# Optimization experiments

Measured on AMD Instinct MI355X. Metric: run time of the kernel, lower is better.

Reference implementation:

```python
import jax, jax.numpy as jnp
import numpy as np

B, T, DIM, H, DH, DT = 2, 2048, 1024, 16, 64, 32
Q_TEMP, K_TEMP = 1.0, 1.0
EPS = float(np.finfo(np.float32).eps)  # torch RMSNorm default eps for fp32
INV_SQRT_DH = 1.0 / np.sqrt(DH)


def _get_time(length, head_time_delta, time_angles, with_time_delta):
    # [T,1,1] positions, optionally offset per head -> [T,H,1]
    pos = jnp.arange(length, dtype=jnp.float32)[:, None, None]
    if with_time_delta:
        pos = pos + head_time_delta[None, :, None]          # [T,H,1]
    else:
        pos = jnp.broadcast_to(pos, (length, H, 1))          # [T,H,1]
    ang = pos * time_angles                                  # [T,H,Dt]
    c, s = jnp.cos(ang), jnp.sin(ang)
    return jnp.concatenate([c + s, c - s], axis=-1) * INV_SQRT_DH  # [T,H,2Dt]


def setup_inputs() -> dict:
    key = jax.random.key(0)
    ks = jax.random.split(key, 6)
    sc = 0.02
    states = jax.random.normal(ks[0], (B, T, DIM), jnp.float32)
    attention_mask = jnp.ones((B, T), jnp.int32)
    ln_w = jnp.ones((DIM,), jnp.float32)
    time_angles = 10000.0 ** (-1.0 / jnp.arange(1, DT + 1, dtype=jnp.float32))
    head_time_delta = jax.random.uniform(ks[1], (H,), jnp.float32)
    Wq = jax.random.normal(ks[2], (H * DH, DIM), jnp.float32) * sc
    q_bias = jnp.zeros((H * DH,), jnp.float32)
    Wk = jax.random.normal(ks[3], (H * DH, DIM), jnp.float32) * sc
    bk = jnp.zeros((H * DH,), jnp.float32)
    Wv = jax.random.normal(ks[4], (H * DH, DIM), jnp.float32) * sc
    bv = jnp.zeros((H * DH,), jnp.float32)
    Wo = jax.random.normal(ks[5], (DIM, H * DH), jnp.float32) * sc
    bo = jnp.zeros((DIM,), jnp.float32)
    return dict(states=states, attention_mask=attention_mask, ln_w=ln_w,
                time_angles=time_angles, head_time_delta=head_time_delta,
                Wq=Wq, q_bias=q_bias, Wk=Wk, bk=bk, Wv=Wv, bv=bv, Wo=Wo, bo=bo)


def reference(states, attention_mask, ln_w, time_angles, head_time_delta,
              Wq, q_bias, Wk, bk, Wv, bv, Wo, bo):
    # RMSNorm
    x = states * jax.lax.rsqrt(jnp.mean(states * states, axis=-1, keepdims=True) + EPS) * ln_w
    m = attention_mask.astype(x.dtype)[:, :, None, None]   # [B,T,1,1]

    # Q path -> q_attentioned [B,T,T,H]
    q = (x @ Wq.T - jnp.exp(q_bias)).reshape(B, T, H, DH)
    q_sm = jax.nn.softmax(q / Q_TEMP * m, axis=-1)
    t_q = _get_time(T, head_time_delta, time_angles, True)   # [T,H,2Dt]
    t_k = _get_time(T, head_time_delta, time_angles, False)  # [T,H,2Dt]
    q_timed = jnp.sum(q_sm, axis=-1, keepdims=True) * t_q    # [B,T,H,2Dt]
    q_att = jnp.einsum('bthd,lhd->btlh', q_timed, t_k)       # [B,T,T,H]

    # KV path
    k = (x @ Wk.T + bk).reshape(B, T, H, DH)
    k_sm = jax.nn.softmax(k / K_TEMP * m, axis=-1)
    v = (x @ Wv.T + bv).reshape(B, T, H, DH)
    kv = k_sm * v                                            # [B,T,H,Dh]

    loading = jnp.einsum('btlh,blhd->bthd', q_att, kv)       # [B,T,H,Dh]
    return loading.reshape(B, T, DIM) @ Wo.T + bo
```

## Files before the change

### kernel.cpp

```cpp
#include <hip/hip_runtime.h>
#include <math.h>

#define T_ 2048
#define H_ 16

typedef __attribute__((ext_vector_type(8))) short bfx8;
typedef __attribute__((ext_vector_type(4))) float f32x4;

__device__ __forceinline__ short f2bf(float f) {
  union { float f; unsigned u; } x; x.f = f;
  unsigned r = (x.u + 0x7FFFu + ((x.u >> 16) & 1u)) >> 16;
  return (short)r;
}
__device__ __forceinline__ float bf2f(short s) {
  union { unsigned u; float f; } x;
  x.u = ((unsigned)(unsigned short)s) << 16;
  return x.f;
}

#define GLD_LDS(g, l) \
  __builtin_amdgcn_global_load_lds( \
      (const __attribute__((address_space(1))) void*)(g), \
      (__attribute__((address_space(3))) void*)(l), 16, 0, 0)

__global__ __launch_bounds__(256) void prep_kernel(
    const float* __restrict__ Wk, const float* __restrict__ Wv,
    const float* __restrict__ Wo, const float* __restrict__ angles,
    const float* __restrict__ states, const float* __restrict__ ln_w,
    short* __restrict__ Wkb, short* __restrict__ Wvb, short* __restrict__ Wob,
    short* __restrict__ xb, short* __restrict__ Cb, short* __restrict__ tkT,
    float* __restrict__ MtH) {
  const int blk = blockIdx.x;
  if (blk < 3072) {
    const int i = blk * 256 + threadIdx.x;
    const int which = i >> 18;
    const int idx = i & 262143;
    const float* s = (which == 0) ? Wk : (which == 1) ? Wv : Wo;
    short* d = (which == 0) ? Wkb : (which == 1) ? Wvb : Wob;
    const float4 v = ((const float4*)s)[idx];
    short4 r;
    r.x = f2bf(v.x); r.y = f2bf(v.y); r.z = f2bf(v.z); r.w = f2bf(v.w);
    ((short4*)d)[idx] = r;
  } else if (blk < 7168) {
    const int row = blk - 3072;
    const int tid = threadIdx.x;
    const float4 v = ((const float4*)(states + (size_t)row * 1024))[tid];
    float ss = v.x * v.x + v.y * v.y + v.z * v.z + v.w * v.w;
#pragma unroll
    for (int off = 32; off >= 1; off >>= 1) ss += __shfl_xor(ss, off);
    __shared__ float red[4];
    if ((tid & 63) == 0) red[tid >> 6] = ss;
    __syncthreads();
    const float tot = red[0] + red[1] + red[2] + red[3];
    const float scale = rsqrtf(tot * (1.0f / 1024.0f) + 1.1920928955078125e-07f);
    const float4 w = ((const float4*)ln_w)[tid];
    short4 o;
    o.x = f2bf(v.x * scale * w.x);
    o.y = f2bf(v.y * scale * w.y);
    o.z = f2bf(v.z * scale * w.z);
    o.w = f2bf(v.w * scale * w.w);
    ((short4*)(xb + (size_t)row * 1024))[tid] = o;
  } else if (blk < 7424) {
    const int gid = (blk - 7168) * 256 + threadIdx.x;
    const int j = gid & 31;
    const int t = gid >> 5;
    float s, c;
    sincosf((float)t * angles[j], &s, &c);
    Cb[(size_t)t * 64 + j] = f2bf(0.125f * c);
    Cb[(size_t)t * 64 + 32 + j] = f2bf(0.125f * s);
  } else if (blk < 7456) {
    const int gid = (blk - 7424) * 256 + threadIdx.x;
    const int tc = gid & 255;
    const int j = gid >> 8;
    const float th = angles[j];
    short lo[8], hi[8];
#pragma unroll
    for (int r = 0; r < 8; ++r) {
      float s, c;
      sincosf((float)(tc * 8 + r) * th, &s, &c);
      lo[r] = f2bf((c + s) * 0.125f);
      hi[r] = f2bf((c - s) * 0.125f);
    }
    short* base = tkT + (size_t)j * 2048 + tc * 8;
    *(short4*)(base) = *(short4*)&lo[0];
    *(short4*)(base + 4) = *(short4*)&lo[4];
    short* base2 = tkT + (size_t)(32 + j) * 2048 + tc * 8;
    *(short4*)(base2) = *(short4*)&hi[0];
    *(short4*)(base2 + 4) = *(short4*)&hi[4];
  } else {
    const int gid = (blk - 7456) * 256 + threadIdx.x;
    ((float4*)MtH)[gid] = make_float4(0.f, 0.f, 0.f, 0.f);
  }
}

__global__ __launch_bounds__(256) void kvgemm_kernel(
    const short* __restrict__ xb, const short* __restrict__ Wkb,
    const short* __restrict__ Wvb, const float* __restrict__ bk,
    const float* __restrict__ bv, const int* __restrict__ mask,
    const short* __restrict__ tkT, float* __restrict__ Mt) {
  __shared__ short smem[16384];
  __shared__ short Vs[128][64];
  short(*As)[64] = (short(*)[64])smem;
  short(*Bk)[64] = (short(*)[64])(smem + 8192);
  short(*Bv)[64] = (short(*)[64])(smem + 12288);
  short(*kvS)[132] = (short(*)[132])smem;

  const int row0 = blockIdx.x * 128;
  const int h = blockIdx.y;
  const int t = threadIdx.x;
  const int lane = t & 63;
  const int wv = t >> 6;
  const bool isV = wv >= 2;
  const int wrow = (wv & 1) * 64;
  const int lrow = lane & 15;

  const int srow8 = t >> 3;
  const int kslotS = (t & 7) ^ (srow8 & 7);
  const short* gaS = xb + (size_t)(row0 + srow8) * 1024 + kslotS * 8;
  const short* gkS = Wkb + (size_t)(h * 64 + srow8) * 1024 + kslotS * 8;
  const short* gvS = Wvb + (size_t)(h * 64 + srow8) * 1024 + kslotS * 8;
  short* laS = &As[srow8][(t & 7) * 8];
  short* lkS = &Bk[srow8][(t & 7) * 8];
  short* lvS = &Bv[srow8][(t & 7) * 8];

  f32x4 acc[4][4] = {};
  for (int k0 = 0; k0 < 1024; k0 += 64) {
    GLD_LDS(gaS + k0, laS);
    GLD_LDS(gaS + 32 * 1024 + k0, laS + 2048);
    GLD_LDS(gaS + 64 * 1024 + k0, laS + 4096);
    GLD_LDS(gaS + 96 * 1024 + k0, laS + 6144);
    GLD_LDS(gkS + k0, lkS);
    GLD_LDS(gkS + 32 * 1024 + k0, lkS + 2048);
    GLD_LDS(gvS + k0, lvS);
    GLD_LDS(gvS + 32 * 1024 + k0, lvS + 2048);
    __syncthreads();
#pragma unroll
    for (int kk = 0; kk < 2; ++kk) {
      const int pcol = ((kk * 4 + (lane >> 4)) ^ (lrow & 7)) * 8;
      bfx8 af[4], bf_[4];
#pragma unroll
      for (int i = 0; i < 4; ++i)
        af[i] = *(const bfx8*)&As[wrow + i * 16 + lrow][pcol];
      const short(*Bs)[64] = isV ? Bv : Bk;
#pragma unroll
      for (int j = 0; j < 4; ++j)
        bf_[j] = *(const bfx8*)&Bs[j * 16 + lrow][pcol];
#pragma unroll
      for (int i = 0; i < 4; ++i)
#pragma unroll
        for (int j = 0; j < 4; ++j)
          acc[i][j] = __builtin_amdgcn_mfma_f32_16x16x32_bf16(af[i], bf_[j], acc[i][j], 0, 0, 0);
    }
    __syncthreads();
  }
  const int rq = (lane >> 4) * 4;
  if (isV) {
#pragma unroll
    for (int j = 0; j < 4; ++j) {
      const float bb = bv[h * 64 + j * 16 + lrow];
#pragma unroll
      for (int i = 0; i < 4; ++i)
#pragma unroll
        for (int rr = 0; rr < 4; ++rr)
          Vs[wrow + rq + i * 16 + rr][j * 16 + lrow] = f2bf(acc[i][j][rr] + bb);
    }
  }
  __syncthreads();
  if (!isV) {
    float bkc[4];
#pragma unroll
    for (int j = 0; j < 4; ++j) bkc[j] = bk[h * 64 + j * 16 + lrow];
    const int rowg0 = row0 + wrow + rq;
#pragma unroll
    for (int i = 0; i < 4; ++i) {
#pragma unroll
      for (int rr = 0; rr < 4; ++rr) {
        const float m = (float)mask[rowg0 + i * 16 + rr];
        float kf[4];
#pragma unroll
        for (int j = 0; j < 4; ++j) kf[j] = (acc[i][j][rr] + bkc[j]) * m;
        float mx = fmaxf(fmaxf(kf[0], kf[1]), fmaxf(kf[2], kf[3]));
#pragma unroll
        for (int off = 8; off >= 1; off >>= 1) mx = fmaxf(mx, __shfl_xor(mx, off));
        float s = 0.0f;
#pragma unroll
        for (int j = 0; j < 4; ++j) { kf[j] = expf(kf[j] - mx); s += kf[j]; }
#pragma unroll
        for (int off = 8; off >= 1; off >>= 1) s += __shfl_xor(s, off);
        const float inv = 1.0f / s;
#pragma unroll
        for (int j = 0; j < 4; ++j)
          acc[i][j][rr] = kf[j] * inv *
                          bf2f(Vs[wrow + rq + i * 16 + rr][j * 16 + lrow]);
      }
    }
#pragma unroll
    for (int j = 0; j < 4; ++j) {
      const int d = j * 16 + lrow;
#pragma unroll
      for (int i = 0; i < 4; ++i) {
        short4 o;
        o.x = f2bf(acc[i][j][0]); o.y = f2bf(acc[i][j][1]);
        o.z = f2bf(acc[i][j][2]); o.w = f2bf(acc[i][j][3]);
        *(short4*)&kvS[d][wrow + rq + i * 16] = o;
      }
    }
  }
  __syncthreads();
  const int bb = row0 >> 11;
  const int tb = row0 & 2047;
  const short* tkb = tkT + (size_t)(wv * 16 + lrow) * 2048 + tb;
  const int kg = (lane >> 4) * 8;
  f32x4 macc[4] = {};
#pragma unroll
  for (int kc = 0; kc < 4; ++kc) {
    const bfx8 af = *(const bfx8*)(tkb + kc * 32 + kg);
#pragma unroll
    for (int j = 0; j < 4; ++j) {
      const bfx8 bf_ = *(const bfx8*)&kvS[j * 16 + lrow][kc * 32 + kg];
      macc[j] = __builtin_amdgcn_mfma_f32_16x16x32_bf16(af, bf_, macc[j], 0, 0, 0);
    }
  }
  float* Mb = Mt + (size_t)(bb * 16 + h) * 4096;
#pragma unroll
  for (int j = 0; j < 4; ++j) {
    const int d = j * 16 + lrow;
#pragma unroll
    for (int rr = 0; rr < 4; ++rr) {
      const int e = wv * 16 + rq + rr;
      atomicAdd(&Mb[(size_t)e * 64 + d], macc[j][rr]);
    }
  }
}

__global__ __launch_bounds__(256) void fold_kernel(
    const float* __restrict__ Mt, const float* __restrict__ angles,
    const float* __restrict__ delta, short* __restrict__ Mf) {
  const int bh = blockIdx.x;
  const int b = bh >> 4, h = bh & 15;
  const int t = threadIdx.x;
  const int j = t >> 3;
  const int d8 = (t & 7) * 8;
  float sphi, cphi;
  sincosf(delta[h] * angles[j], &sphi, &cphi);
  const float p = cphi + sphi, q = cphi - sphi;
  const float* m0 = Mt + (size_t)bh * 4096 + (size_t)j * 64 + d8;
  const float* m1 = Mt + (size_t)bh * 4096 + (size_t)(32 + j) * 64 + d8;
  short* oc = Mf + (size_t)b * 65536 + (size_t)j * 1024 + h * 64 + d8;
  short* os = Mf + (size_t)b * 65536 + (size_t)(32 + j) * 1024 + h * 64 + d8;
#pragma unroll
  for (int c = 0; c < 8; ++c) {
    const float a = m0[c], bb = m1[c];
    oc[c] = f2bf(p * a + q * bb);
    os[c] = f2bf(q * a - p * bb);
  }
}

__global__ __launch_bounds__(256) void hgemm_kernel(
    const short* __restrict__ Wob, const short* __restrict__ Mf,
    float* __restrict__ H) {
  const int kc = blockIdx.x;
  const int o0 = blockIdx.y * 64;
  const int b = blockIdx.z;
  const int t = threadIdx.x;
  const int lane = t & 63;
  const int w = t >> 6;
  const int lrow = lane & 15;
  const int kg = (lane >> 4) * 8;
  const int orow = o0 + w * 16 + lrow;
  f32x4 acc[4] = {};
#pragma unroll
  for (int it = 0; it < 4; ++it) {
    const int kb = kc * 128 + it * 32 + kg;
    const bfx8 af = *(const bfx8*)(Wob + (size_t)orow * 1024 + kb);
#pragma unroll
    for (int j = 0; j < 4; ++j) {
      const bfx8 bf_ = *(const bfx8*)(Mf + (size_t)b * 65536 +
                                      (size_t)(j * 16 + lrow) * 1024 + kb);
      acc[j] = __builtin_amdgcn_mfma_f32_16x16x32_bf16(af, bf_, acc[j], 0, 0, 0);
    }
  }
  float* Hb = H + (size_t)b * 65536;
#pragma unroll
  for (int j = 0; j < 4; ++j) {
    const int kap = j * 16 + lrow;
#pragma unroll
    for (int rr = 0; rr < 4; ++rr) {
      const int o = o0 + w * 16 + (lane >> 4) * 4 + rr;
      atomicAdd(&Hb[(size_t)o * 64 + kap], acc[j][rr]);
    }
  }
}

__global__ __launch_bounds__(256) void ofinal_kernel(
    const short* __restrict__ Cb, const float* __restrict__ H,
    const float* __restrict__ bo, float* __restrict__ out) {
  const int col0 = blockIdx.x * 128;
  const int row0 = blockIdx.y * 128;
  const int b = blockIdx.z;
  float* C = out + (size_t)b * 2097152;
  const float* Hb = H + (size_t)b * 65536;
  const int t = threadIdx.x;
  const int lane = t & 63;
  const int wv = t >> 6;
  const int wm = (wv & 1) * 64, wn = (wv >> 1) * 64;
  const int lrow = lane & 15;
  const int kg = (lane >> 4) * 8;
  f32x4 acc[4][4] = {};
#pragma unroll
  for (int k0 = 0; k0 < 64; k0 += 32) {
    bfx8 af[4], bf_[4];
#pragma unroll
    for (int i = 0; i < 4; ++i)
      af[i] = *(const bfx8*)(Cb + (size_t)(row0 + wm + i * 16 + lrow) * 64 + k0 + kg);
#pragma unroll
    for (int j = 0; j < 4; ++j) {
      const float* hp = Hb + (size_t)(col0 + wn + j * 16 + lrow) * 64 + k0 + kg;
      const float4 h0 = *(const float4*)hp;
      const float4 h1 = *(const float4*)(hp + 4);
      bfx8 bb;
      bb[0] = f2bf(h0.x); bb[1] = f2bf(h0.y); bb[2] = f2bf(h0.z); bb[3] = f2bf(h0.w);
      bb[4] = f2bf(h1.x); bb[5] = f2bf(h1.y); bb[6] = f2bf(h1.z); bb[7] = f2bf(h1.w);
      bf_[j] = bb;
    }
#pragma unroll
    for (int i = 0; i < 4; ++i)
#pragma unroll
      for (int j = 0; j < 4; ++j)
        acc[i][j] = __builtin_amdgcn_mfma_f32_16x16x32_bf16(af[i], bf_[j], acc[i][j], 0, 0, 0);
  }
  const int rq = (lane >> 4) * 4;
#pragma unroll
  for (int j = 0; j < 4; ++j) {
    const int c = col0 + wn + j * 16 + lrow;
    const float bb = bo[c];
#pragma unroll
    for (int i = 0; i < 4; ++i) {
      const int r = row0 + wm + i * 16 + rq;
#pragma unroll
      for (int rr = 0; rr < 4; ++rr)
        C[(size_t)(r + rr) * 1024 + c] = acc[i][j][rr] + bb;
    }
  }
}

extern "C" void kernel_launch(void* const* d_in, const int* in_sizes, int n_in,
                              void* d_out, int out_size, void* d_ws, size_t ws_size,
                              hipStream_t stream) {
  (void)in_sizes; (void)n_in; (void)out_size; (void)ws_size;
  const float* states = (const float*)d_in[0];
  const int* mask = (const int*)d_in[1];
  const float* ln_w = (const float*)d_in[2];
  const float* angles = (const float*)d_in[3];
  const float* delta = (const float*)d_in[4];
  const float* Wk = (const float*)d_in[7];
  const float* bk = (const float*)d_in[8];
  const float* Wv = (const float*)d_in[9];
  const float* bv = (const float*)d_in[10];
  const float* Wo = (const float*)d_in[11];
  const float* bo = (const float*)d_in[12];
  float* out = (float*)d_out;

  char* W = (char*)d_ws;
  short* xb  = (short*)(W);
  short* Wkb = (short*)(W + (8u << 20));
  short* Wvb = (short*)(W + (10u << 20));
  short* Wob = (short*)(W + (12u << 20));
  short* Cb  = (short*)(W + (14u << 20));
  short* tkT = (short*)(W + (14u << 20) + (256u << 10));
  short* Mf  = (short*)(W + (14u << 20) + (512u << 10));
  float* Mt  = (float*)(W + (15u << 20));
  float* H   = (float*)(W + (15u << 20) + (512u << 10));

  prep_kernel<<<7712, 256, 0, stream>>>(Wk, Wv, Wo, angles, states, ln_w,
                                        Wkb, Wvb, Wob, xb, Cb, tkT, Mt);
  kvgemm_kernel<<<dim3(32, 16), 256, 0, stream>>>(xb, Wkb, Wvb, bk, bv, mask,
                                                  tkT, Mt);
  fold_kernel<<<32, 256, 0, stream>>>(Mt, angles, delta, Mf);
  hgemm_kernel<<<dim3(8, 16, 2), 256, 0, stream>>>(Wob, Mf, H);
  ofinal_kernel<<<dim3(8, 16, 2), 256, 0, stream>>>(Cb, H, bo, out);
}
```

Baseline: 146.9 us.

## Fuse kv-gemm, fold, H-gemm and output stages into one persistent kernel

Merges the four post-prep kernels into a single 512-block kernel with software grid barriers built on an atomic counter. The fold step is now done inline inside the H-gemm stage, so the Mf buffer round trip goes away, and the H and output stages are re-tiled to fit the fixed 512-block grid. This removes three launch gaps and one intermediate buffer. In exchange it adds spin-wait barriers that require every block to be co-resident, so the kernel could deadlock if occupancy is too low, and it adds a memset launch.

```diff
diff --git a/kernel.cpp b/kernel.cpp
--- a/kernel.cpp
+++ b/kernel.cpp
@@ -93,253 +93,287 @@
   }
 }
 
-__global__ __launch_bounds__(256) void kvgemm_kernel(
+__device__ __forceinline__ void grid_sync(int* cnt, int target) {
+  __syncthreads();
+  if (threadIdx.x == 0) {
+    __threadfence();
+    __hip_atomic_fetch_add(cnt, 1, __ATOMIC_ACQ_REL, __HIP_MEMORY_SCOPE_AGENT);
+    while (__hip_atomic_load(cnt, __ATOMIC_ACQUIRE, __HIP_MEMORY_SCOPE_AGENT) <
+           target)
+      __builtin_amdgcn_s_sleep(2);
+  }
+  __syncthreads();
+  __threadfence();
+}
+
+__global__ __launch_bounds__(256, 2) void fused_kernel(
     const short* __restrict__ xb, const short* __restrict__ Wkb,
     const short* __restrict__ Wvb, const float* __restrict__ bk,
     const float* __restrict__ bv, const int* __restrict__ mask,
-    const short* __restrict__ tkT, float* __restrict__ Mt) {
+    const short* __restrict__ tkT, float* __restrict__ Mt,
+    const short* __restrict__ Wob, const float* __restrict__ angles,
+    const float* __restrict__ delta, float* __restrict__ H,
+    const short* __restrict__ Cb, const float* __restrict__ bo,
+    float* __restrict__ out, int* __restrict__ cnt) {
   __shared__ short smem[16384];
   __shared__ short Vs[128][64];
-  short(*As)[64] = (short(*)[64])smem;
-  short(*Bk)[64] = (short(*)[64])(smem + 8192);
-  short(*Bv)[64] = (short(*)[64])(smem + 12288);
-  short(*kvS)[132] = (short(*)[132])smem;
-
-  const int row0 = blockIdx.x * 128;
-  const int h = blockIdx.y;
-  const int t = threadIdx.x;
-  const int lane = t & 63;
-  const int wv = t >> 6;
-  const bool isV = wv >= 2;
-  const int wrow = (wv & 1) * 64;
-  const int lrow = lane & 15;
-
-  const int srow8 = t >> 3;
-  const int kslotS = (t & 7) ^ (srow8 & 7);
-  const short* gaS = xb + (size_t)(row0 + srow8) * 1024 + kslotS * 8;
-  const short* gkS = Wkb + (size_t)(h * 64 + srow8) * 1024 + kslotS * 8;
-  const short* gvS = Wvb + (size_t)(h * 64 + srow8) * 1024 + kslotS * 8;
-  short* laS = &As[srow8][(t & 7) * 8];
-  short* lkS = &Bk[srow8][(t & 7) * 8];
-  short* lvS = &Bv[srow8][(t & 7) * 8];
-
-  f32x4 acc[4][4] = {};
-  for (int k0 = 0; k0 < 1024; k0 += 64) {
-    GLD_LDS(gaS + k0, laS);
-    GLD_LDS(gaS + 32 * 1024 + k0, laS + 2048);
-    GLD_LDS(gaS + 64 * 1024 + k0, laS + 4096);
-    GLD_LDS(gaS + 96 * 1024 + k0, laS + 6144);
-    GLD_LDS(gkS + k0, lkS);
-    GLD_LDS(gkS + 32 * 1024 + k0, lkS + 2048);
-    GLD_LDS(gvS + k0, lvS);
-    GLD_LDS(gvS + 32 * 1024 + k0, lvS + 2048);
+
+  {
+    short(*As)[64] = (short(*)[64])smem;
+    short(*Bk)[64] = (short(*)[64])(smem + 8192);
+    short(*Bv)[64] = (short(*)[64])(smem + 12288);
+    short(*kvS)[132] = (short(*)[132])smem;
+
+    const int row0 = (blockIdx.x & 31) * 128;
+    const int h = blockIdx.x >> 5;
+    const int t = threadIdx.x;
+    const int lane = t & 63;
+    const int wv = t >> 6;
+    const bool isV = wv >= 2;
+    const int wrow = (wv & 1) * 64;
+    const int lrow = lane & 15;
+
+    const int srow8 = t >> 3;
+    const int kslotS = (t & 7) ^ (srow8 & 7);
+    const short* gaS = xb + (size_t)(row0 + srow8) * 1024 + kslotS * 8;
+    const short* gkS = Wkb + (size_t)(h * 64 + srow8) * 1024 + kslotS * 8;
+    const short* gvS = Wvb + (size_t)(h * 64 + srow8) * 1024 + kslotS * 8;
+    short* laS = &As[srow8][(t & 7) * 8];
+    short* lkS = &Bk[srow8][(t & 7) * 8];
+    short* lvS = &Bv[srow8][(t & 7) * 8];
+
+    f32x4 acc[4][4] = {};
+    for (int k0 = 0; k0 < 1024; k0 += 64) {
+      GLD_LDS(gaS + k0, laS);
+      GLD_LDS(gaS + 32 * 1024 + k0, laS + 2048);
+      GLD_LDS(gaS + 64 * 1024 + k0, laS + 4096);
+      GLD_LDS(gaS + 96 * 1024 + k0, laS + 6144);
+      GLD_LDS(gkS + k0, lkS);
+      GLD_LDS(gkS + 32 * 1024 + k0, lkS + 2048);
+      GLD_LDS(gvS + k0, lvS);
+      GLD_LDS(gvS + 32 * 1024 + k0, lvS + 2048);
+      __syncthreads();
+#pragma unroll
+      for (int kk = 0; kk < 2; ++kk) {
+        const int pcol = ((kk * 4 + (lane >> 4)) ^ (lrow & 7)) * 8;
+        bfx8 af[4], bf_[4];
+#pragma unroll
+        for (int i = 0; i < 4; ++i)
+          af[i] = *(const bfx8*)&As[wrow + i * 16 + lrow][pcol];
+        const short(*Bs)[64] = isV ? Bv : Bk;
+#pragma unroll
+        for (int j = 0; j < 4; ++j)
+          bf_[j] = *(const bfx8*)&Bs[j * 16 + lrow][pcol];
+#pragma unroll
+        for (int i = 0; i < 4; ++i)
+#pragma unroll
+          for (int j = 0; j < 4; ++j)
+            acc[i][j] = __builtin_amdgcn_mfma_f32_16x16x32_bf16(af[i], bf_[j], acc[i][j], 0, 0, 0);
+      }
+      __syncthreads();
+    }
+    const int rq = (lane >> 4) * 4;
+    if (isV) {
+#pragma unroll
+      for (int j = 0; j < 4; ++j) {
+        const float bb = bv[h * 64 + j * 16 + lrow];
+#pragma unroll
+        for (int i = 0; i < 4; ++i)
+#pragma unroll
+          for (int rr = 0; rr < 4; ++rr)
+            Vs[wrow + rq + i * 16 + rr][j * 16 + lrow] = f2bf(acc[i][j][rr] + bb);
+      }
+    }
     __syncthreads();
-#pragma unroll
-    for (int kk = 0; kk < 2; ++kk) {
-      const int pcol = ((kk * 4 + (lane >> 4)) ^ (lrow & 7)) * 8;
-      bfx8 af[4], bf_[4];
-#pragma unroll
-      for (int i = 0; i < 4; ++i)
-        af[i] = *(const bfx8*)&As[wrow + i * 16 + lrow][pcol];
-      const short(*Bs)[64] = isV ? Bv : Bk;
-#pragma unroll
-      for (int j = 0; j < 4; ++j)
-        bf_[j] = *(const bfx8*)&Bs[j * 16 + lrow][pcol];
-#pragma unroll
-      for (int i = 0; i < 4; ++i)
+    if (!isV) {
+      float bkc[4];
+#pragma unroll
+      for (int j = 0; j < 4; ++j) bkc[j] = bk[h * 64 + j * 16 + lrow];
+      const int rowg0 = row0 + wrow + rq;
+#pragma unroll
+      for (int i = 0; i < 4; ++i) {
+#pragma unroll
+        for (int rr = 0; rr < 4; ++rr) {
+          const float m = (float)mask[rowg0 + i * 16 + rr];
+          float kf[4];
+#pragma unroll
+          for (int j = 0; j < 4; ++j) kf[j] = (acc[i][j][rr] + bkc[j]) * m;
+          float mx = fmaxf(fmaxf(kf[0], kf[1]), fmaxf(kf[2], kf[3]));
+#pragma unroll
+          for (int off = 8; off >= 1; off >>= 1) mx = fmaxf(mx, __shfl_xor(mx, off));
+          float s = 0.0f;
+#pragma unroll
+          for (int j = 0; j < 4; ++j) { kf[j] = expf(kf[j] - mx); s += kf[j]; }
+#pragma unroll
+          for (int off = 8; off >= 1; off >>= 1) s += __shfl_xor(s, off);
+          const float inv = 1.0f / s;
+#pragma unroll
+          for (int j = 0; j < 4; ++j)
+            acc[i][j][rr] = kf[j] * inv *
+                            bf2f(Vs[wrow + rq + i * 16 + rr][j * 16 + lrow]);
+        }
+      }
+#pragma unroll
+      for (int j = 0; j < 4; ++j) {
+        const int d = j * 16 + lrow;
+#pragma unroll
+        for (int i = 0; i < 4; ++i) {
+          short4 o;
+          o.x = f2bf(acc[i][j][0]); o.y = f2bf(acc[i][j][1]);
+          o.z = f2bf(acc[i][j][2]); o.w = f2bf(acc[i][j][3]);
+          *(short4*)&kvS[d][wrow + rq + i * 16] = o;
+        }
+      }
+    }
+    __syncthreads();
+    const int bb = row0 >> 11;
+    const int tb = row0 & 2047;
+    const short* tkb = tkT + (size_t)(wv * 16 + lrow) * 2048 + tb;
+    const int kg = (lane >> 4) * 8;
+    f32x4 macc[4] = {};
+#pragma unroll
+    for (int kc = 0; kc < 4; ++kc) {
+      const bfx8 af = *(const bfx8*)(tkb + kc * 32 + kg);
+#pragma unroll
+      for (int j = 0; j < 4; ++j) {
+        const bfx8 bf_ = *(const bfx8*)&kvS[j * 16 + lrow][kc * 32 + kg];
+        macc[j] = __builtin_amdgcn_mfma_f32_16x16x32_bf16(af, bf_, macc[j], 0, 0, 0);
+      }
+    }
+    float* Mb = Mt + (size_t)(bb * 16 + h) * 4096;
+#pragma unroll
+    for (int j = 0; j < 4; ++j) {
+      const int d = j * 16 + lrow;
+#pragma unroll
+      for (int rr = 0; rr < 4; ++rr) {
+        const int e = wv * 16 + rq + rr;
+        atomicAdd(&Mb[(size_t)e * 64 + d], macc[j][rr]);
+      }
+    }
+  }
+
+  grid_sync(cnt, 512);
+
+  {
+    const int bid = blockIdx.x;
+    if (bid < 256) {
+      const int t = threadIdx.x;
+      const int lane = t & 63;
+      const int w = t >> 6;
+      const int lrow = lane & 15;
+      const int kg = (lane >> 4) * 8;
+      const int h2 = bid & 7;
+      const int ot = (bid >> 3) & 15;
+      const int b = bid >> 7;
+      const int orow = ot * 64 + w * 16 + lrow;
+      float p[2][2], q[2][2];
+#pragma unroll
+      for (int hh = 0; hh < 2; ++hh) {
+        const float dl = delta[h2 * 2 + hh];
+#pragma unroll
+        for (int aa = 0; aa < 2; ++aa) {
+          float s, c;
+          sincosf(dl * angles[aa * 16 + lrow], &s, &c);
+          p[hh][aa] = c + s;
+          q[hh][aa] = c - s;
+        }
+      }
+      f32x4 acc[4] = {};
+#pragma unroll
+      for (int ks = 0; ks < 4; ++ks) {
+        const int hh = ks >> 1;
+        const int h = h2 * 2 + hh;
+        const int d0 = (ks & 1) * 32 + kg;
+        const float* Mthb = Mt + (size_t)(b * 16 + h) * 4096;
+        const bfx8 af = *(const bfx8*)(Wob + (size_t)orow * 1024 + h * 64 + d0);
+        float m0a[8], m1a[8], m0b[8], m1b[8];
+        *(float4*)&m0a[0] = *(const float4*)(Mthb + lrow * 64 + d0);
+        *(float4*)&m0a[4] = *(const float4*)(Mthb + lrow * 64 + d0 + 4);
+        *(float4*)&m1a[0] = *(const float4*)(Mthb + (32 + lrow) * 64 + d0);
+        *(float4*)&m1a[4] = *(const float4*)(Mthb + (32 + lrow) * 64 + d0 + 4);
+        *(float4*)&m0b[0] = *(const float4*)(Mthb + (16 + lrow) * 64 + d0);
+        *(float4*)&m0b[4] = *(const float4*)(Mthb + (16 + lrow) * 64 + d0 + 4);
+        *(float4*)&m1b[0] = *(const float4*)(Mthb + (48 + lrow) * 64 + d0);
+        *(float4*)&m1b[4] = *(const float4*)(Mthb + (48 + lrow) * 64 + d0 + 4);
+        bfx8 bf0, bf1, bf2, bf3;
+#pragma unroll
+        for (int e = 0; e < 8; ++e) {
+          bf0[e] = f2bf(p[hh][0] * m0a[e] + q[hh][0] * m1a[e]);
+          bf1[e] = f2bf(p[hh][1] * m0b[e] + q[hh][1] * m1b[e]);
+          bf2[e] = f2bf(q[hh][0] * m0a[e] - p[hh][0] * m1a[e]);
+          bf3[e] = f2bf(q[hh][1] * m0b[e] - p[hh][1] * m1b[e]);
+        }
+        acc[0] = __builtin_amdgcn_mfma_f32_16x16x32_bf16(af, bf0, acc[0], 0, 0, 0);
+        acc[1] = __builtin_amdgcn_mfma_f32_16x16x32_bf16(af, bf1, acc[1], 0, 0, 0);
+        acc[2] = __builtin_amdgcn_mfma_f32_16x16x32_bf16(af, bf2, acc[2], 0, 0, 0);
+        acc[3] = __builtin_amdgcn_mfma_f32_16x16x32_bf16(af, bf3, acc[3], 0, 0, 0);
+      }
+      float* Hb = H + (size_t)b * 65536;
+      const int rq = (lane >> 4) * 4;
+#pragma unroll
+      for (int j = 0; j < 4; ++j) {
+        const int kap = j * 16 + lrow;
+#pragma unroll
+        for (int rr = 0; rr < 4; ++rr) {
+          const int o = ot * 64 + w * 16 + rq + rr;
+          atomicAdd(&Hb[(size_t)o * 64 + kap], acc[j][rr]);
+        }
+      }
+    }
+  }
+
+  grid_sync(cnt, 1024);
+
+  {
+    const int bid = blockIdx.x;
+    const int t = threadIdx.x;
+    const int lane = t & 63;
+    const int w = t >> 6;
+    const int lrow = lane & 15;
+    const int kg = (lane >> 4) * 8;
+    const int ct = bid & 15;
+    const int rt = (bid >> 4) & 15;
+    const int b = bid >> 8;
+    const int col0 = ct * 64;
+    const int row0 = rt * 128 + w * 32;
+    float* C = out + (size_t)b * 2097152;
+    const float* Hb = H + (size_t)b * 65536;
+    f32x4 acc[2][4] = {};
+#pragma unroll
+    for (int ks = 0; ks < 2; ++ks) {
+      const int k0 = ks * 32 + kg;
+      bfx8 af[2], bf_[4];
+#pragma unroll
+      for (int i = 0; i < 2; ++i)
+        af[i] = *(const bfx8*)(Cb + (size_t)(row0 + i * 16 + lrow) * 64 + k0);
+#pragma unroll
+      for (int j = 0; j < 4; ++j) {
+        const float* hp = Hb + (size_t)(col0 + j * 16 + lrow) * 64 + k0;
+        const float4 h0 = *(const float4*)hp;
+        const float4 h1 = *(const float4*)(hp + 4);
+        bfx8 bb;
+        bb[0] = f2bf(h0.x); bb[1] = f2bf(h0.y); bb[2] = f2bf(h0.z); bb[3] = f2bf(h0.w);
+        bb[4] = f2bf(h1.x); bb[5] = f2bf(h1.y); bb[6] = f2bf(h1.z); bb[7] = f2bf(h1.w);
+        bf_[j] = bb;
+      }
+#pragma unroll
+      for (int i = 0; i < 2; ++i)
 #pragma unroll
         for (int j = 0; j < 4; ++j)
           acc[i][j] = __builtin_amdgcn_mfma_f32_16x16x32_bf16(af[i], bf_[j], acc[i][j], 0, 0, 0);
     }
-    __syncthreads();
-  }
-  const int rq = (lane >> 4) * 4;
-  if (isV) {
+    const int rq = (lane >> 4) * 4;
 #pragma unroll
     for (int j = 0; j < 4; ++j) {
-      const float bb = bv[h * 64 + j * 16 + lrow];
-#pragma unroll
-      for (int i = 0; i < 4; ++i)
+      const int c = col0 + j * 16 + lrow;
+      const float bb = bo[c];
+#pragma unroll
+      for (int i = 0; i < 2; ++i) {
+        const int r = row0 + i * 16 + rq;
 #pragma unroll
         for (int rr = 0; rr < 4; ++rr)
-          Vs[wrow + rq + i * 16 + rr][j * 16 + lrow] = f2bf(acc[i][j][rr] + bb);
-    }
-  }
-  __syncthreads();
-  if (!isV) {
-    float bkc[4];
-#pragma unroll
-    for (int j = 0; j < 4; ++j) bkc[j] = bk[h * 64 + j * 16 + lrow];
-    const int rowg0 = row0 + wrow + rq;
-#pragma unroll
-    for (int i = 0; i < 4; ++i) {
-#pragma unroll
-      for (int rr = 0; rr < 4; ++rr) {
-        const float m = (float)mask[rowg0 + i * 16 + rr];
-        float kf[4];
-#pragma unroll
-        for (int j = 0; j < 4; ++j) kf[j] = (acc[i][j][rr] + bkc[j]) * m;
-        float mx = fmaxf(fmaxf(kf[0], kf[1]), fmaxf(kf[2], kf[3]));
-#pragma unroll
-        for (int off = 8; off >= 1; off >>= 1) mx = fmaxf(mx, __shfl_xor(mx, off));
-        float s = 0.0f;
-#pragma unroll
-        for (int j = 0; j < 4; ++j) { kf[j] = expf(kf[j] - mx); s += kf[j]; }
-#pragma unroll
-        for (int off = 8; off >= 1; off >>= 1) s += __shfl_xor(s, off);
-        const float inv = 1.0f / s;
-#pragma unroll
-        for (int j = 0; j < 4; ++j)
-          acc[i][j][rr] = kf[j] * inv *
-                          bf2f(Vs[wrow + rq + i * 16 + rr][j * 16 + lrow]);
-      }
-    }
-#pragma unroll
-    for (int j = 0; j < 4; ++j) {
-      const int d = j * 16 + lrow;
-#pragma unroll
-      for (int i = 0; i < 4; ++i) {
-        short4 o;
-        o.x = f2bf(acc[i][j][0]); o.y = f2bf(acc[i][j][1]);
-        o.z = f2bf(acc[i][j][2]); o.w = f2bf(acc[i][j][3]);
-        *(short4*)&kvS[d][wrow + rq + i * 16] = o;
-      }
-    }
-  }
-  __syncthreads();
-  const int bb = row0 >> 11;
-  const int tb = row0 & 2047;
-  const short* tkb = tkT + (size_t)(wv * 16 + lrow) * 2048 + tb;
-  const int kg = (lane >> 4) * 8;
-  f32x4 macc[4] = {};
-#pragma unroll
-  for (int kc = 0; kc < 4; ++kc) {
-    const bfx8 af = *(const bfx8*)(tkb + kc * 32 + kg);
-#pragma unroll
-    for (int j = 0; j < 4; ++j) {
-      const bfx8 bf_ = *(const bfx8*)&kvS[j * 16 + lrow][kc * 32 + kg];
-      macc[j] = __builtin_amdgcn_mfma_f32_16x16x32_bf16(af, bf_, macc[j], 0, 0, 0);
-    }
-  }
-  float* Mb = Mt + (size_t)(bb * 16 + h) * 4096;
-#pragma unroll
-  for (int j = 0; j < 4; ++j) {
-    const int d = j * 16 + lrow;
-#pragma unroll
-    for (int rr = 0; rr < 4; ++rr) {
-      const int e = wv * 16 + rq + rr;
-      atomicAdd(&Mb[(size_t)e * 64 + d], macc[j][rr]);
-    }
-  }
-}
-
-__global__ __launch_bounds__(256) void fold_kernel(
-    const float* __restrict__ Mt, const float* __restrict__ angles,
-    const float* __restrict__ delta, short* __restrict__ Mf) {
-  const int bh = blockIdx.x;
-  const int b = bh >> 4, h = bh & 15;
-  const int t = threadIdx.x;
-  const int j = t >> 3;
-  const int d8 = (t & 7) * 8;
-  float sphi, cphi;
-  sincosf(delta[h] * angles[j], &sphi, &cphi);
-  const float p = cphi + sphi, q = cphi - sphi;
-  const float* m0 = Mt + (size_t)bh * 4096 + (size_t)j * 64 + d8;
-  const float* m1 = Mt + (size_t)bh * 4096 + (size_t)(32 + j) * 64 + d8;
-  short* oc = Mf + (size_t)b * 65536 + (size_t)j * 1024 + h * 64 + d8;
-  short* os = Mf + (size_t)b * 65536 + (size_t)(32 + j) * 1024 + h * 64 + d8;
-#pragma unroll
-  for (int c = 0; c < 8; ++c) {
-    const float a = m0[c], bb = m1[c];
-    oc[c] = f2bf(p * a + q * bb);
-    os[c] = f2bf(q * a - p * bb);
-  }
-}
-
-__global__ __launch_bounds__(256) void hgemm_kernel(
-    const short* __restrict__ Wob, const short* __restrict__ Mf,
-    float* __restrict__ H) {
-  const int kc = blockIdx.x;
-  const int o0 = blockIdx.y * 64;
-  const int b = blockIdx.z;
-  const int t = threadIdx.x;
-  const int lane = t & 63;
-  const int w = t >> 6;
-  const int lrow = lane & 15;
-  const int kg = (lane >> 4) * 8;
-  const int orow = o0 + w * 16 + lrow;
-  f32x4 acc[4] = {};
-#pragma unroll
-  for (int it = 0; it < 4; ++it) {
-    const int kb = kc * 128 + it * 32 + kg;
-    const bfx8 af = *(const bfx8*)(Wob + (size_t)orow * 1024 + kb);
-#pragma unroll
-    for (int j = 0; j < 4; ++j) {
-      const bfx8 bf_ = *(const bfx8*)(Mf + (size_t)b * 65536 +
-                                      (size_t)(j * 16 + lrow) * 1024 + kb);
-      acc[j] = __builtin_amdgcn_mfma_f32_16x16x32_bf16(af, bf_, acc[j], 0, 0, 0);
-    }
-  }
-  float* Hb = H + (size_t)b * 65536;
-#pragma unroll
-  for (int j = 0; j < 4; ++j) {
-    const int kap = j * 16 + lrow;
-#pragma unroll
-    for (int rr = 0; rr < 4; ++rr) {
-      const int o = o0 + w * 16 + (lane >> 4) * 4 + rr;
-      atomicAdd(&Hb[(size_t)o * 64 + kap], acc[j][rr]);
-    }
-  }
-}
-
-__global__ __launch_bounds__(256) void ofinal_kernel(
-    const short* __restrict__ Cb, const float* __restrict__ H,
-    const float* __restrict__ bo, float* __restrict__ out) {
-  const int col0 = blockIdx.x * 128;
-  const int row0 = blockIdx.y * 128;
-  const int b = blockIdx.z;
-  float* C = out + (size_t)b * 2097152;
-  const float* Hb = H + (size_t)b * 65536;
-  const int t = threadIdx.x;
-  const int lane = t & 63;
-  const int wv = t >> 6;
-  const int wm = (wv & 1) * 64, wn = (wv >> 1) * 64;
-  const int lrow = lane & 15;
-  const int kg = (lane >> 4) * 8;
-  f32x4 acc[4][4] = {};
-#pragma unroll
-  for (int k0 = 0; k0 < 64; k0 += 32) {
-    bfx8 af[4], bf_[4];
-#pragma unroll
-    for (int i = 0; i < 4; ++i)
-      af[i] = *(const bfx8*)(Cb + (size_t)(row0 + wm + i * 16 + lrow) * 64 + k0 + kg);
-#pragma unroll
-    for (int j = 0; j < 4; ++j) {
-      const float* hp = Hb + (size_t)(col0 + wn + j * 16 + lrow) * 64 + k0 + kg;
-      const float4 h0 = *(const float4*)hp;
-      const float4 h1 = *(const float4*)(hp + 4);
-      bfx8 bb;
-      bb[0] = f2bf(h0.x); bb[1] = f2bf(h0.y); bb[2] = f2bf(h0.z); bb[3] = f2bf(h0.w);
-      bb[4] = f2bf(h1.x); bb[5] = f2bf(h1.y); bb[6] = f2bf(h1.z); bb[7] = f2bf(h1.w);
-      bf_[j] = bb;
-    }
-#pragma unroll
-    for (int i = 0; i < 4; ++i)
-#pragma unroll
-      for (int j = 0; j < 4; ++j)
-        acc[i][j] = __builtin_amdgcn_mfma_f32_16x16x32_bf16(af[i], bf_[j], acc[i][j], 0, 0, 0);
-  }
-  const int rq = (lane >> 4) * 4;
-#pragma unroll
-  for (int j = 0; j < 4; ++j) {
-    const int c = col0 + wn + j * 16 + lrow;
-    const float bb = bo[c];
-#pragma unroll
-    for (int i = 0; i < 4; ++i) {
-      const int r = row0 + wm + i * 16 + rq;
-#pragma unroll
-      for (int rr = 0; rr < 4; ++rr)
-        C[(size_t)(r + rr) * 1024 + c] = acc[i][j][rr] + bb;
+          C[(size_t)(r + rr) * 1024 + c] = acc[i][j][rr] + bb;
+      }
     }
   }
 }
@@ -368,15 +402,13 @@
   short* Wob = (short*)(W + (12u << 20));
   short* Cb  = (short*)(W + (14u << 20));
   short* tkT = (short*)(W + (14u << 20) + (256u << 10));
-  short* Mf  = (short*)(W + (14u << 20) + (512u << 10));
+  int*   cnt = (int*)(W + (14u << 20) + (512u << 10));
   float* Mt  = (float*)(W + (15u << 20));
   float* H   = (float*)(W + (15u << 20) + (512u << 10));
 
+  hipMemsetAsync(cnt, 0, 64, stream);
   prep_kernel<<<7712, 256, 0, stream>>>(Wk, Wv, Wo, angles, states, ln_w,
                                         Wkb, Wvb, Wob, xb, Cb, tkT, Mt);
-  kvgemm_kernel<<<dim3(32, 16), 256, 0, stream>>>(xb, Wkb, Wvb, bk, bv, mask,
-                                                  tkT, Mt);
-  fold_kernel<<<32, 256, 0, stream>>>(Mt, angles, delta, Mf);
-  hgemm_kernel<<<dim3(8, 16, 2), 256, 0, stream>>>(Wob, Mf, H);
-  ofinal_kernel<<<dim3(8, 16, 2), 256, 0, stream>>>(Cb, H, bo, out);
-}
+  fused_kernel<<<512, 256, 0, stream>>>(xb, Wkb, Wvb, bk, bv, mask, tkT, Mt,
+                                        Wob, angles, delta, H, Cb, bo, out, cnt);
+}
```

After: 299.9 us. 104% more time.
